# Kernel optimization log

Hardware: AMD Instinct MI355X
Metric: run time of the kernel (lower is better)

The kernel has to match this reference:

```python
import jax, jax.numpy as jnp
import numpy as np

TRACE_LR = 0.1
TRACE_DECAY = 0.99
ERASE_LR = 1.0
EPS = 1e-8


def setup_inputs() -> dict:
    key = jax.random.key(0)
    k1, k2, k3, k4 = jax.random.split(key, 4)
    B, H, S, D = 8, 8, 4096, 64
    DM = 768
    Q = jax.random.normal(k1, (B, H, S, D), dtype=jnp.float32)
    V = jax.random.normal(k2, (B, H, S, D), dtype=jnp.float32)
    # value_traces buffer (small random state so erase path is non-trivial)
    trace = jax.random.normal(k3, (H, D, D), dtype=jnp.float32) * 0.01
    # W_out: Linear(H*D -> DM), weight shape (DM, H*D), out = x @ W.T
    W_out = jax.random.normal(k4, (DM, H * D), dtype=jnp.float32) / np.sqrt(H * D)
    return {"Q": Q, "V": V, "trace": trace, "W_out": W_out}


def _hebbian_write(Q, V, trace):
    """Erase-before-write + decayed Hebbian outer-product update.

    Q, V: (B, H, S, D); trace: (H, D, D). Shift-1 offset: key at i, value at i+2.
    """
    B, H, S, D = Q.shape
    Q_store = Q[:, :, :-2, :]            # (B,H,S-2,D)
    V_store = V[:, :, 2:, :]             # (B,H,S-2,D)
    denom = B * (S - 2)
    # reconsolidation erasure of old associations along normalized keys
    Q_norm = jnp.clip(jnp.linalg.norm(Q_store, axis=-1, keepdims=True), EPS)
    Q_erase = Q_store / Q_norm
    V_old = jnp.einsum('bhip,hpq->bhiq', Q_erase, trace)
    erase = jnp.einsum('bhip,bhiq->hpq', Q_erase, V_old) / denom
    trace = trace - ERASE_LR * erase
    # Hebbian outer-product write
    update = jnp.einsum('bhip,bhiq->hpq', Q_store, V_store) / denom
    return TRACE_DECAY * trace + TRACE_LR * update


def reference(Q, V, trace, W_out):
    B, H, S, D = Q.shape
    new_trace = _hebbian_write(Q, V, trace)
    # shift-1 retrieval: Q_addr at position i uses Q from position i-1
    Q_addr = jnp.concatenate(
        [jnp.zeros_like(Q[:, :, :1, :]), Q[:, :, :-1, :]], axis=2)  # (B,H,S,D)
    V_ret = jnp.einsum('bhsp,hpq->bhsq', Q_addr, new_trace)          # (B,H,S,D)
    V_ret = V_ret.transpose(0, 2, 1, 3).reshape(B, S, H * D)         # (B,S,H*D)
    return V_ret @ W_out.T                                           # (B,S,d_model)
```

## Files before the change

### kernel.cpp

```cpp
#include <hip/hip_runtime.h>

#define B_ 8
#define H_ 8
#define S_ 4096
#define D_ 64
#define DM_ 768
#define NSTORE 4094
#define DENOM 32752.0f

typedef short bfrag_t __attribute__((ext_vector_type(8)));
typedef float f32x4_t __attribute__((ext_vector_type(4)));

__device__ inline unsigned short f2bf(float x) {
    unsigned int u = __float_as_uint(x);
    unsigned int r = (u + 0x7fffu + ((u >> 16) & 1u)) >> 16;
    return (unsigned short)r;
}

__device__ inline unsigned int cvtpk(float lo, float hi) {
    unsigned int r;
    asm("v_cvt_pk_bf16_f32 %0, %1, %2" : "=v"(r) : "v"(lo), "v"(hi));
    return r;
}

__device__ inline void pl16swap(float& a, float& b) {
    asm("v_permlane16_swap_b32 %0, %1" : "+v"(a), "+v"(b));
}
__device__ inline void pl32swap(float& a, float& b) {
    asm("v_permlane32_swap_b32 %0, %1" : "+v"(a), "+v"(b));
}

template <int CTRL>
__device__ inline float dpp_add(float x) {
    int y = __builtin_amdgcn_update_dpp(0, __float_as_int(x), CTRL, 0xf, 0xf, true);
    return x + __int_as_float(y);
}

__device__ inline void async_copy16(const void* g, void* lds) {
    __builtin_amdgcn_global_load_lds((__attribute__((address_space(1))) void*)g,
                                     (__attribute__((address_space(3))) void*)lds,
                                     16, 0, 0);
}

__device__ inline void barrier_lds_only() {
    __builtin_amdgcn_sched_barrier(0);
    asm volatile("s_waitcnt lgkmcnt(0)" ::: "memory");
    __builtin_amdgcn_s_barrier();
    __builtin_amdgcn_sched_barrier(0);
}

#define MFMA16(a, b, c) __builtin_amdgcn_mfma_f32_16x16x32_bf16((a), (b), (c), 0, 0, 0)

template <bool PART>
__global__ __launch_bounds__(256, 4) void gram_kernel(
    const float* __restrict__ Q, const float* __restrict__ V,
    float* __restrict__ gG, float* __restrict__ gU,
    unsigned short* __restrict__ Qbf, float* __restrict__ gP, int writeQbf) {
    const int split = blockIdx.x, h = blockIdx.y, b = blockIdx.z;
    const int nsplit = gridDim.x;
    const int rowsPer = 4096 / nsplit;
    const int nTiles = rowsPer >> 6;
    const int tmask = nTiles - 1;
    const int t = threadIdx.x;
    const int wave = t >> 6, lane = t & 63;
    const int quad = lane >> 4, l15 = lane & 15;
    const int rgrp = t >> 4;
    const int c4 = t & 15;
    __shared__ __align__(16) unsigned short Qs[2][4096];
    __shared__ __align__(16) unsigned short Vs[2][4096];

    const size_t bh = (size_t)(b * H_ + h);
    const float* Qbh = Q + bh * S_ * D_;
    const float* Vbh = V + bh * S_ * D_;
    unsigned short* Qo = Qbf + bh * S_ * D_;

    f32x4_t accG[4] = {}, accU[4] = {};
    const int r0 = split * rowsPer;

    float4 qr[4], vr[4];
    auto loadT = [&](int tile) {
        const int rbase = r0 + tile * 64;
        #pragma unroll
        for (int i = 0; i < 4; ++i) {
            int r = rbase + i * 16 + rgrp;
            qr[i] = *(const float4*)(Qbh + (size_t)r * D_ + c4 * 4);
            vr[i] = (r < NSTORE) ? *(const float4*)(Vbh + (size_t)(r + 2) * D_ + c4 * 4)
                                 : make_float4(0.f, 0.f, 0.f, 0.f);
        }
    };
    auto rd8 = [&](const unsigned short* arr, int p, int gk) {
        const int bx = p & 15;
        uint2 lo = *(const uint2*)&arr[p * 64 + (((gk * 2) ^ bx) << 2)];
        uint2 hi = *(const uint2*)&arr[p * 64 + (((gk * 2 + 1) ^ bx) << 2)];
        union { uint2 u2[2]; bfrag_t f; } u;
        u.u2[0] = lo; u.u2[1] = hi;
        return u.f;
    };

    const int tstart = (split * 3 + h * 5 + b * 7) & tmask;

    loadT(tstart);
    for (int it = 0; it < nTiles; ++it) {
        const int tile = (tstart + it) & tmask;
        const int buf = it & 1;
        const int rbase = r0 + tile * 64;
        unsigned short* Qb_ = Qs[buf];
        unsigned short* Vb_ = Vs[buf];
        #pragma unroll
        for (int i = 0; i < 4; ++i) {
            int r = rbase + i * 16 + rgrp;
            float4 q4 = qr[i], v4 = vr[i];
            if (writeQbf) {
                uint2 u = make_uint2(cvtpk(q4.x, q4.y), cvtpk(q4.z, q4.w));
                *(uint2*)(Qo + (size_t)r * D_ + c4 * 4) = u;
            }
            if (r >= NSTORE) q4 = make_float4(0.f, 0.f, 0.f, 0.f);
            float ss = q4.x * q4.x + q4.y * q4.y + q4.z * q4.z + q4.w * q4.w;
            ss = dpp_add<0xB1>(ss);
            ss = dpp_add<0x4E>(ss);
            ss = dpp_add<0x141>(ss);
            ss = dpp_add<0x140>(ss);
            float sc = fmaxf(ss, 1e-16f);
            float sr = rsqrtf(sc);
            float sv = sc * sr;
            float a0 = q4.x * sr, a1 = q4.y * sr, a2 = q4.z * sr, a3 = q4.w * sr;
            float b0 = v4.x * sv, b1 = v4.y * sv, b2 = v4.z * sv, b3 = v4.w * sv;
            pl16swap(a0, a1); pl16swap(a2, a3);
            pl32swap(a0, a2); pl32swap(a1, a3);
            pl16swap(b0, b1); pl16swap(b2, b3);
            pl32swap(b0, b2); pl32swap(b1, b3);
            const int p = c4 * 4 + quad;
            const int off = p * 64 + (((i * 4 + wave) ^ (p & 15)) << 2);
            *(uint2*)&Qb_[off] = make_uint2(cvtpk(a0, a1), cvtpk(a2, a3));
            *(uint2*)&Vb_[off] = make_uint2(cvtpk(b0, b1), cvtpk(b2, b3));
        }
        if (it + 1 < nTiles) loadT((tstart + it + 1) & tmask);
        barrier_lds_only();
        #pragma unroll
        for (int c = 0; c < 2; ++c) {
            const int gk = c * 4 + quad;
            bfrag_t af = rd8(Qb_, wave * 16 + l15, gk);
            #pragma unroll
            for (int j = 0; j < 4; ++j) {
                bfrag_t bq = rd8(Qb_, j * 16 + l15, gk);
                bfrag_t bv = rd8(Vb_, j * 16 + l15, gk);
                accG[j] = MFMA16(af, bq, accG[j]);
                accU[j] = MFMA16(af, bv, accU[j]);
            }
        }
    }
    if (PART) {
        const int slab = split * 8 + b;
        float* base = gP + ((size_t)(h * 128 + slab) * 2) * 4096;
        #pragma unroll
        for (int j = 0; j < 4; ++j) {
            int coln = j * 16 + l15;
            #pragma unroll
            for (int r = 0; r < 4; ++r) {
                int row = wave * 16 + quad * 4 + r;
                base[row * 64 + coln]        = accG[j][r];
                base[4096 + row * 64 + coln] = accU[j][r];
            }
        }
    } else {
        float* gGh = gG + h * 4096;
        float* gUh = gU + h * 4096;
        #pragma unroll
        for (int j = 0; j < 4; ++j) {
            int coln = j * 16 + l15;
            #pragma unroll
            for (int r = 0; r < 4; ++r) {
                int row = wave * 16 + quad * 4 + r;
                atomicAdd(&gGh[row * 64 + coln], accG[j][r]);
                atomicAdd(&gUh[row * 64 + coln], accU[j][r]);
            }
        }
    }
}

__global__ __launch_bounds__(256) void reduce_kernel(
    const float* __restrict__ gP, float* __restrict__ gG, float* __restrict__ gU) {
    const int h = blockIdx.x, chunk = blockIdx.y, t = threadIdx.x;
    const int arr = t >> 7, idx = chunk * 128 + (t & 127);
    const float* base = gP + ((size_t)(h * 128) * 2 + arr) * 4096 + idx;
    const int slstart = ((h << 4) + (chunk << 2)) & 127;
    float s = 0.f;
    #pragma unroll 8
    for (int i = 0; i < 128; ++i) {
        int sl = (slstart + i) & 127;
        s += base[(size_t)sl * 2 * 4096];
    }
    (arr ? gU : gG)[h * 4096 + idx] = s;
}

__global__ __launch_bounds__(256) void wc_kernel(
    const float* __restrict__ gG, const float* __restrict__ gU,
    const float* __restrict__ trace, const float* __restrict__ Wout,
    unsigned short* __restrict__ WcT) {
    const int nc = blockIdx.x, h = blockIdx.y, t = threadIdx.x;
    __shared__ float Gs[64][68];
    __shared__ float Ts[64][68];
    __shared__ float TsT[64][68];
    __shared__ float WbT[64][132];
    const float* Gh = gG + h * 4096;
    const float* Uh = gU + h * 4096;
    const float* Th = trace + h * 4096;
    #pragma unroll
    for (int k = 0; k < 16; ++k) {
        int e = k * 256 + t;
        Gs[e >> 6][e & 63] = Gh[e];
        Ts[e >> 6][e & 63] = Th[e];
    }
    #pragma unroll
    for (int i = 0; i < 8; ++i) {
        int f = i * 256 + t;
        int n = f >> 4, q4 = f & 15;
        float4 w = *(const float4*)(Wout + (size_t)(nc * 128 + n) * 512 + h * 64 + q4 * 4);
        WbT[q4 * 4 + 0][n] = w.x; WbT[q4 * 4 + 1][n] = w.y;
        WbT[q4 * 4 + 2][n] = w.z; WbT[q4 * 4 + 3][n] = w.w;
    }
    __syncthreads();
    {
        const int p = t >> 2, q0 = (t & 3) * 16;
        f32x4_t acc[4] = {};
        for (int r = 0; r < 64; ++r) {
            float g = Gs[p][r];
            #pragma unroll
            for (int i = 0; i < 4; ++i) {
                f32x4_t tv = *(const f32x4_t*)&Ts[r][q0 + i * 4];
                acc[i] += g * tv;
            }
        }
        const float inv = 1.0f / DENOM;
        #pragma unroll
        for (int i = 0; i < 4; ++i) {
            f32x4_t ts = *(const f32x4_t*)&Ts[p][q0 + i * 4];
            f32x4_t uu = *(const f32x4_t*)(Uh + p * 64 + q0 + i * 4);
            f32x4_t res = 0.99f * (ts - acc[i] * inv) + (0.1f * inv) * uu;
            TsT[q0 + i * 4 + 0][p] = res[0];
            TsT[q0 + i * 4 + 1][p] = res[1];
            TsT[q0 + i * 4 + 2][p] = res[2];
            TsT[q0 + i * 4 + 3][p] = res[3];
        }
    }
    __syncthreads();
    const int n0 = (t >> 4) * 8, p0 = (t & 15) * 4;
    f32x4_t acc[8] = {};
    for (int q = 0; q < 64; ++q) {
        f32x4_t tp = *(const f32x4_t*)&TsT[q][p0];
        f32x4_t w0 = *(const f32x4_t*)&WbT[q][n0];
        f32x4_t w1 = *(const f32x4_t*)&WbT[q][n0 + 4];
        #pragma unroll
        for (int i = 0; i < 4; ++i) acc[i] += w0[i] * tp;
        #pragma unroll
        for (int i = 0; i < 4; ++i) acc[4 + i] += w1[i] * tp;
    }
    #pragma unroll
    for (int i = 0; i < 8; ++i) {
        int n = nc * 128 + n0 + i;
        ushort4 u;
        u.x = f2bf(acc[i][0]); u.y = f2bf(acc[i][1]);
        u.z = f2bf(acc[i][2]); u.w = f2bf(acc[i][3]);
        *(ushort4*)(WcT + (size_t)n * 512 + h * 64 + p0) = u;
    }
}

__global__ __launch_bounds__(256, 3) void matmul_fast(
    const unsigned short* __restrict__ Qb, const unsigned short* __restrict__ WcT,
    float* __restrict__ out) {
    const int mTile = blockIdx.x;
    const int nTile = blockIdx.y;
    const int t = threadIdx.x;
    const int wave = t >> 6, lane = t & 63;
    const int wm = wave >> 1, wn = wave & 1;
    const int quad = lane >> 4, l15 = lane & 15;
    __shared__ __align__(16) unsigned short As[128 * 64];
    __shared__ __align__(16) unsigned short Bs[128 * 64];
    const int b = mTile >> 5;
    const int s0 = (mTile & 31) * 128;
    const int nBase = nTile * 128;
    const int rl8 = lane >> 3, g = lane & 7;
    const int gs = g ^ rl8;
    f32x4_t acc[4][4] = {};

    const int hstart = (mTile * 3 + nTile * 5) & 7;
    for (int hh = 0; hh < 8; ++hh) {
        const int h = (hstart + hh) & 7;
        const unsigned short* Qbh = Qb + (size_t)(b * H_ + h) * S_ * D_;
        #pragma unroll
        for (int k = 0; k < 4; ++k) {
            int ch = wave * 4 + k;
            int row = ch * 8 + rl8;
            int s = s0 + row;
            int sc = (s > 0) ? (s - 1) : 0;
            async_copy16(Qbh + (size_t)sc * 64 + gs * 8, &As[ch * 512 + lane * 8]);
            async_copy16(WcT + (size_t)(nBase + row) * 512 + h * 64 + gs * 8,
                         &Bs[ch * 512 + lane * 8]);
        }
        __syncthreads();
        if (s0 == 0) {
            if (t < 8) ((uint4*)As)[t] = make_uint4(0, 0, 0, 0);
            __syncthreads();
        }
        #pragma unroll
        for (int c = 0; c < 2; ++c) {
            int gk = c * 4 + quad;
            bfrag_t af[4], bf[4];
            #pragma unroll
            for (int i = 0; i < 4; ++i) {
                int row = wm * 64 + i * 16 + l15;
                af[i] = *(const bfrag_t*)&As[row * 64 + ((gk ^ (row & 7)) << 3)];
            }
            #pragma unroll
            for (int j = 0; j < 4; ++j) {
                int row = wn * 64 + j * 16 + l15;
                bf[j] = *(const bfrag_t*)&Bs[row * 64 + ((gk ^ (row & 7)) << 3)];
            }
            #pragma unroll
            for (int i = 0; i < 4; ++i)
                #pragma unroll
                for (int j = 0; j < 4; ++j)
                    acc[i][j] = MFMA16(af[i], bf[j], acc[i][j]);
        }
        __syncthreads();
    }
    const size_t mBase = (size_t)mTile * 128;
    #pragma unroll
    for (int i = 0; i < 4; ++i) {
        int mrow = wm * 64 + i * 16 + quad * 4;
        #pragma unroll
        for (int j = 0; j < 4; ++j) {
            int n = nBase + wn * 64 + j * 16 + l15;
            #pragma unroll
            for (int r = 0; r < 4; ++r)
                out[(mBase + mrow + r) * DM_ + n] = acc[i][j][r];
        }
    }
}

__global__ __launch_bounds__(256, 2) void matmul_f32(
    const float* __restrict__ Qf, const unsigned short* __restrict__ WcT,
    float* __restrict__ out) {
    const int mTile = blockIdx.x, nTile = blockIdx.y;
    const int t = threadIdx.x;
    const int wave = t >> 6, lane = t & 63;
    const int wm = wave >> 1, wn = wave & 1;
    const int quad = lane >> 4, l15 = lane & 15;
    __shared__ __align__(16) unsigned short As[128][72];
    __shared__ __align__(16) unsigned short Bs[128][72];
    const int b = mTile >> 5;
    const int s0 = (mTile & 31) * 128;
    const int nBase = nTile * 128;
    f32x4_t acc[4][4] = {};
    const int hstart = (mTile * 3 + nTile * 5) & 7;
    for (int hh = 0; hh < 8; ++hh) {
        const int h = (hstart + hh) & 7;
        const float* Qbh = Qf + (size_t)(b * H_ + h) * S_ * D_;
        #pragma unroll
        for (int i = 0; i < 8; ++i) {
            int f = i * 256 + t;
            int row = f >> 4, c4 = f & 15;
            int s = s0 + row;
            float4 q4 = make_float4(0.f, 0.f, 0.f, 0.f);
            if (s > 0) q4 = *(const float4*)(Qbh + (size_t)(s - 1) * D_ + c4 * 4);
            ushort4 u;
            u.x = f2bf(q4.x); u.y = f2bf(q4.y); u.z = f2bf(q4.z); u.w = f2bf(q4.w);
            *(ushort4*)(&As[row][c4 * 4]) = u;
        }
        #pragma unroll
        for (int i = 0; i < 4; ++i) {
            int f = i * 256 + t;
            int row = f >> 3, c8 = f & 7;
            uint4 w = *(const uint4*)(WcT + (size_t)(nBase + row) * 512 + h * 64 + c8 * 8);
            *(uint4*)(&Bs[row][c8 * 8]) = w;
        }
        __syncthreads();
        #pragma unroll
        for (int c = 0; c < 2; ++c) {
            int k0 = c * 32 + quad * 8;
            bfrag_t af[4], bf[4];
            #pragma unroll
            for (int i = 0; i < 4; ++i)
                af[i] = *(const bfrag_t*)(&As[wm * 64 + i * 16 + l15][k0]);
            #pragma unroll
            for (int j = 0; j < 4; ++j)
                bf[j] = *(const bfrag_t*)(&Bs[wn * 64 + j * 16 + l15][k0]);
            #pragma unroll
            for (int i = 0; i < 4; ++i)
                #pragma unroll
                for (int j = 0; j < 4; ++j)
                    acc[i][j] = MFMA16(af[i], bf[j], acc[i][j]);
        }
        __syncthreads();
    }
    const size_t mBase = (size_t)mTile * 128;
    #pragma unroll
    for (int i = 0; i < 4; ++i) {
        int mrow = wm * 64 + i * 16 + quad * 4;
        #pragma unroll
        for (int j = 0; j < 4; ++j) {
            int n = nBase + wn * 64 + j * 16 + l15;
            #pragma unroll
            for (int r = 0; r < 4; ++r)
                out[(mBase + mrow + r) * DM_ + n] = acc[i][j][r];
        }
    }
}

extern "C" void kernel_launch(void* const* d_in, const int* in_sizes, int n_in,
                              void* d_out, int out_size, void* d_ws, size_t ws_size,
                              hipStream_t stream) {
    const float* Q     = (const float*)d_in[0];
    const float* V     = (const float*)d_in[1];
    const float* trace = (const float*)d_in[2];
    const float* Wout  = (const float*)d_in[3];
    float* out = (float*)d_out;

    float* gG   = (float*)d_ws;
    float* gU   = gG + 32768;
    float* Tnew = gU + 32768;
    unsigned short* WcT = (unsigned short*)(Tnew + 32768);
    unsigned short* Qbf = WcT + 393216;
    float* gP = (float*)(Qbf + (size_t)B_ * H_ * S_ * D_);

    const size_t needQbf  = 1179648u + 33554432u;
    const size_t needFull = needQbf + 33554432u;
    const int mode = (ws_size >= needFull) ? 2 : ((ws_size >= needQbf) ? 1 : 0);

    if (mode == 2) {
        gram_kernel<true><<<dim3(16, 8, 8), 256, 0, stream>>>(Q, V, gG, gU, Qbf, gP, 1);
        reduce_kernel<<<dim3(8, 32), 256, 0, stream>>>(gP, gG, gU);
    } else {
        hipMemsetAsync(d_ws, 0, 2 * 32768 * sizeof(float), stream);
        gram_kernel<false><<<dim3(8, 8, 8), 256, 0, stream>>>(Q, V, gG, gU, Qbf, gP, mode >= 1);
    }
    wc_kernel<<<dim3(6, 8), 256, 0, stream>>>(gG, gU, trace, Wout, WcT);
    if (mode >= 1)
        matmul_fast<<<dim3(256, 6), 256, 0, stream>>>(Qbf, WcT, out);
    else
        matmul_f32<<<dim3(256, 6), 256, 0, stream>>>(Q, WcT, out);
}
```

Baseline: 265.5 us.

## Drop partial-slab reduction; single-buffer gram kernel with more splits and atomics

Removes the partial-sum workspace path and its separate reduce kernel, so the Gram and update matrices are always accumulated with global atomics after a memset. The gram kernel loses its register prefetch and LDS double buffering: it loads each tile directly and adds a second barrier per tile. It now runs 32 splits per (b,h) with a launch bound raised to 6 blocks per CU. The aim is to hide latency through occupancy instead of software pipelining and to drop the extra kernel and its traffic, at the price of more atomic contention and exposed load latency.

```diff
diff --git a/kernel.cpp b/kernel.cpp
--- a/kernel.cpp
+++ b/kernel.cpp
@@ -51,11 +51,10 @@
 
 #define MFMA16(a, b, c) __builtin_amdgcn_mfma_f32_16x16x32_bf16((a), (b), (c), 0, 0, 0)
 
-template <bool PART>
-__global__ __launch_bounds__(256, 4) void gram_kernel(
+__global__ __launch_bounds__(256, 6) void gram_kernel(
     const float* __restrict__ Q, const float* __restrict__ V,
     float* __restrict__ gG, float* __restrict__ gU,
-    unsigned short* __restrict__ Qbf, float* __restrict__ gP, int writeQbf) {
+    unsigned short* __restrict__ Qbf, int writeQbf) {
     const int split = blockIdx.x, h = blockIdx.y, b = blockIdx.z;
     const int nsplit = gridDim.x;
     const int rowsPer = 4096 / nsplit;
@@ -66,8 +65,8 @@
     const int quad = lane >> 4, l15 = lane & 15;
     const int rgrp = t >> 4;
     const int c4 = t & 15;
-    __shared__ __align__(16) unsigned short Qs[2][4096];
-    __shared__ __align__(16) unsigned short Vs[2][4096];
+    __shared__ __align__(16) unsigned short Qs[4096];
+    __shared__ __align__(16) unsigned short Vs[4096];
 
     const size_t bh = (size_t)(b * H_ + h);
     const float* Qbh = Q + bh * S_ * D_;
@@ -77,17 +76,6 @@
     f32x4_t accG[4] = {}, accU[4] = {};
     const int r0 = split * rowsPer;
 
-    float4 qr[4], vr[4];
-    auto loadT = [&](int tile) {
-        const int rbase = r0 + tile * 64;
-        #pragma unroll
-        for (int i = 0; i < 4; ++i) {
-            int r = rbase + i * 16 + rgrp;
-            qr[i] = *(const float4*)(Qbh + (size_t)r * D_ + c4 * 4);
-            vr[i] = (r < NSTORE) ? *(const float4*)(Vbh + (size_t)(r + 2) * D_ + c4 * 4)
-                                 : make_float4(0.f, 0.f, 0.f, 0.f);
-        }
-    };
     auto rd8 = [&](const unsigned short* arr, int p, int gk) {
         const int bx = p & 15;
         uint2 lo = *(const uint2*)&arr[p * 64 + (((gk * 2) ^ bx) << 2)];
@@ -99,17 +87,16 @@
 
     const int tstart = (split * 3 + h * 5 + b * 7) & tmask;
 
-    loadT(tstart);
     for (int it = 0; it < nTiles; ++it) {
         const int tile = (tstart + it) & tmask;
-        const int buf = it & 1;
         const int rbase = r0 + tile * 64;
-        unsigned short* Qb_ = Qs[buf];
-        unsigned short* Vb_ = Vs[buf];
         #pragma unroll
         for (int i = 0; i < 4; ++i) {
             int r = rbase + i * 16 + rgrp;
-            float4 q4 = qr[i], v4 = vr[i];
+            float4 q4 = *(const float4*)(Qbh + (size_t)r * D_ + c4 * 4);
+            float4 v4 = (r < NSTORE)
+                ? *(const float4*)(Vbh + (size_t)(r + 2) * D_ + c4 * 4)
+                : make_float4(0.f, 0.f, 0.f, 0.f);
             if (writeQbf) {
                 uint2 u = make_uint2(cvtpk(q4.x, q4.y), cvtpk(q4.z, q4.w));
                 *(uint2*)(Qo + (size_t)r * D_ + c4 * 4) = u;
@@ -131,66 +118,36 @@
             pl32swap(b0, b2); pl32swap(b1, b3);
             const int p = c4 * 4 + quad;
             const int off = p * 64 + (((i * 4 + wave) ^ (p & 15)) << 2);
-            *(uint2*)&Qb_[off] = make_uint2(cvtpk(a0, a1), cvtpk(a2, a3));
-            *(uint2*)&Vb_[off] = make_uint2(cvtpk(b0, b1), cvtpk(b2, b3));
-        }
-        if (it + 1 < nTiles) loadT((tstart + it + 1) & tmask);
+            *(uint2*)&Qs[off] = make_uint2(cvtpk(a0, a1), cvtpk(a2, a3));
+            *(uint2*)&Vs[off] = make_uint2(cvtpk(b0, b1), cvtpk(b2, b3));
+        }
         barrier_lds_only();
         #pragma unroll
         for (int c = 0; c < 2; ++c) {
             const int gk = c * 4 + quad;
-            bfrag_t af = rd8(Qb_, wave * 16 + l15, gk);
+            bfrag_t af = rd8(Qs, wave * 16 + l15, gk);
             #pragma unroll
             for (int j = 0; j < 4; ++j) {
-                bfrag_t bq = rd8(Qb_, j * 16 + l15, gk);
-                bfrag_t bv = rd8(Vb_, j * 16 + l15, gk);
+                bfrag_t bq = rd8(Qs, j * 16 + l15, gk);
+                bfrag_t bv = rd8(Vs, j * 16 + l15, gk);
                 accG[j] = MFMA16(af, bq, accG[j]);
                 accU[j] = MFMA16(af, bv, accU[j]);
             }
         }
-    }
-    if (PART) {
-        const int slab = split * 8 + b;
-        float* base = gP + ((size_t)(h * 128 + slab) * 2) * 4096;
-        #pragma unroll
-        for (int j = 0; j < 4; ++j) {
-            int coln = j * 16 + l15;
-            #pragma unroll
-            for (int r = 0; r < 4; ++r) {
-                int row = wave * 16 + quad * 4 + r;
-                base[row * 64 + coln]        = accG[j][r];
-                base[4096 + row * 64 + coln] = accU[j][r];
-            }
-        }
-    } else {
-        float* gGh = gG + h * 4096;
-        float* gUh = gU + h * 4096;
-        #pragma unroll
-        for (int j = 0; j < 4; ++j) {
-            int coln = j * 16 + l15;
-            #pragma unroll
-            for (int r = 0; r < 4; ++r) {
-                int row = wave * 16 + quad * 4 + r;
-                atomicAdd(&gGh[row * 64 + coln], accG[j][r]);
-                atomicAdd(&gUh[row * 64 + coln], accU[j][r]);
-            }
-        }
-    }
-}
-
-__global__ __launch_bounds__(256) void reduce_kernel(
-    const float* __restrict__ gP, float* __restrict__ gG, float* __restrict__ gU) {
-    const int h = blockIdx.x, chunk = blockIdx.y, t = threadIdx.x;
-    const int arr = t >> 7, idx = chunk * 128 + (t & 127);
-    const float* base = gP + ((size_t)(h * 128) * 2 + arr) * 4096 + idx;
-    const int slstart = ((h << 4) + (chunk << 2)) & 127;
-    float s = 0.f;
-    #pragma unroll 8
-    for (int i = 0; i < 128; ++i) {
-        int sl = (slstart + i) & 127;
-        s += base[(size_t)sl * 2 * 4096];
-    }
-    (arr ? gU : gG)[h * 4096 + idx] = s;
+        barrier_lds_only();
+    }
+    float* gGh = gG + h * 4096;
+    float* gUh = gU + h * 4096;
+    #pragma unroll
+    for (int j = 0; j < 4; ++j) {
+        int coln = j * 16 + l15;
+        #pragma unroll
+        for (int r = 0; r < 4; ++r) {
+            int row = wave * 16 + quad * 4 + r;
+            atomicAdd(&gGh[row * 64 + coln], accG[j][r]);
+            atomicAdd(&gUh[row * 64 + coln], accU[j][r]);
+        }
+    }
 }
 
 __global__ __launch_bounds__(256) void wc_kernel(
@@ -418,22 +375,15 @@
 
     float* gG   = (float*)d_ws;
     float* gU   = gG + 32768;
-    float* Tnew = gU + 32768;
-    unsigned short* WcT = (unsigned short*)(Tnew + 32768);
+    float* hole = gU + 32768;
+    unsigned short* WcT = (unsigned short*)(hole + 32768);
     unsigned short* Qbf = WcT + 393216;
-    float* gP = (float*)(Qbf + (size_t)B_ * H_ * S_ * D_);
-
-    const size_t needQbf  = 1179648u + 33554432u;
-    const size_t needFull = needQbf + 33554432u;
-    const int mode = (ws_size >= needFull) ? 2 : ((ws_size >= needQbf) ? 1 : 0);
-
-    if (mode == 2) {
-        gram_kernel<true><<<dim3(16, 8, 8), 256, 0, stream>>>(Q, V, gG, gU, Qbf, gP, 1);
-        reduce_kernel<<<dim3(8, 32), 256, 0, stream>>>(gP, gG, gU);
-    } else {
-        hipMemsetAsync(d_ws, 0, 2 * 32768 * sizeof(float), stream);
-        gram_kernel<false><<<dim3(8, 8, 8), 256, 0, stream>>>(Q, V, gG, gU, Qbf, gP, mode >= 1);
-    }
+
+    const size_t needQbf = 1179648u + 33554432u;
+    const int mode = (ws_size >= needQbf) ? 1 : 0;
+
+    hipMemsetAsync(d_ws, 0, 2 * 32768 * sizeof(float), stream);
+    gram_kernel<<<dim3(32, 8, 8), 256, 0, stream>>>(Q, V, gG, gU, Qbf, mode);
     wc_kernel<<<dim3(6, 8), 256, 0, stream>>>(gG, gU, trace, Wout, WcT);
     if (mode >= 1)
         matmul_fast<<<dim3(256, 6), 256, 0, stream>>>(Qbf, WcT, out);
```

Result: slower. 288.3 us (+8.6%).

## Double-buffer matmul_fast LDS tiles and source zero row from a zeroed buffer

Applied to the files above, without the earlier changes.

matmul_fast now keeps two LDS buffers for the A and B tiles and issues the async global-to-LDS copy for the next head while the current head's MFMAs run. The extra barrier that zeroed the first row is removed by pointing the copy at a small zeroed workspace region instead. This doubles LDS use and lowers the launch-bounds occupancy hint from 3 to 2 blocks, and it adds one small memset per launch.

```diff
diff --git a/kernel.cpp b/kernel.cpp
--- a/kernel.cpp
+++ b/kernel.cpp
@@ -45,6 +45,13 @@
 __device__ inline void barrier_lds_only() {
     __builtin_amdgcn_sched_barrier(0);
     asm volatile("s_waitcnt lgkmcnt(0)" ::: "memory");
+    __builtin_amdgcn_s_barrier();
+    __builtin_amdgcn_sched_barrier(0);
+}
+
+__device__ inline void barrier_vm_drain() {
+    __builtin_amdgcn_sched_barrier(0);
+    asm volatile("s_waitcnt vmcnt(0) lgkmcnt(0)" ::: "memory");
     __builtin_amdgcn_s_barrier();
     __builtin_amdgcn_sched_barrier(0);
 }
@@ -104,8 +111,8 @@
         const int tile = (tstart + it) & tmask;
         const int buf = it & 1;
         const int rbase = r0 + tile * 64;
-        unsigned short* Qb_ = Qs[buf];
-        unsigned short* Vb_ = Vs[buf];
+        unsigned short* Qlds = Qs[buf];
+        unsigned short* Vlds = Vs[buf];
         #pragma unroll
         for (int i = 0; i < 4; ++i) {
             int r = rbase + i * 16 + rgrp;
@@ -131,19 +138,19 @@
             pl32swap(b0, b2); pl32swap(b1, b3);
             const int p = c4 * 4 + quad;
             const int off = p * 64 + (((i * 4 + wave) ^ (p & 15)) << 2);
-            *(uint2*)&Qb_[off] = make_uint2(cvtpk(a0, a1), cvtpk(a2, a3));
-            *(uint2*)&Vb_[off] = make_uint2(cvtpk(b0, b1), cvtpk(b2, b3));
+            *(uint2*)&Qlds[off] = make_uint2(cvtpk(a0, a1), cvtpk(a2, a3));
+            *(uint2*)&Vlds[off] = make_uint2(cvtpk(b0, b1), cvtpk(b2, b3));
         }
         if (it + 1 < nTiles) loadT((tstart + it + 1) & tmask);
         barrier_lds_only();
         #pragma unroll
         for (int c = 0; c < 2; ++c) {
             const int gk = c * 4 + quad;
-            bfrag_t af = rd8(Qb_, wave * 16 + l15, gk);
+            bfrag_t af = rd8(Qlds, wave * 16 + l15, gk);
             #pragma unroll
             for (int j = 0; j < 4; ++j) {
-                bfrag_t bq = rd8(Qb_, j * 16 + l15, gk);
-                bfrag_t bv = rd8(Vb_, j * 16 + l15, gk);
+                bfrag_t bq = rd8(Qlds, j * 16 + l15, gk);
+                bfrag_t bv = rd8(Vlds, j * 16 + l15, gk);
                 accG[j] = MFMA16(af, bq, accG[j]);
                 accU[j] = MFMA16(af, bv, accU[j]);
             }
@@ -265,43 +272,52 @@
     }
 }
 
-__global__ __launch_bounds__(256, 3) void matmul_fast(
+__global__ __launch_bounds__(256, 2) void matmul_fast(
     const unsigned short* __restrict__ Qb, const unsigned short* __restrict__ WcT,
-    float* __restrict__ out) {
+    const unsigned short* __restrict__ zeroSrc, float* __restrict__ out) {
     const int mTile = blockIdx.x;
     const int nTile = blockIdx.y;
     const int t = threadIdx.x;
     const int wave = t >> 6, lane = t & 63;
     const int wm = wave >> 1, wn = wave & 1;
     const int quad = lane >> 4, l15 = lane & 15;
-    __shared__ __align__(16) unsigned short As[128 * 64];
-    __shared__ __align__(16) unsigned short Bs[128 * 64];
+    __shared__ __align__(16) unsigned short As[2][128 * 64];
+    __shared__ __align__(16) unsigned short Bs[2][128 * 64];
     const int b = mTile >> 5;
     const int s0 = (mTile & 31) * 128;
     const int nBase = nTile * 128;
     const int rl8 = lane >> 3, g = lane & 7;
     const int gs = g ^ rl8;
     f32x4_t acc[4][4] = {};
-
     const int hstart = (mTile * 3 + nTile * 5) & 7;
-    for (int hh = 0; hh < 8; ++hh) {
+
+    auto stage = [&](int hh, int buf) {
         const int h = (hstart + hh) & 7;
         const unsigned short* Qbh = Qb + (size_t)(b * H_ + h) * S_ * D_;
+        unsigned short* Ap = &As[buf][0];
+        unsigned short* Bp = &Bs[buf][0];
         #pragma unroll
         for (int k = 0; k < 4; ++k) {
             int ch = wave * 4 + k;
             int row = ch * 8 + rl8;
             int s = s0 + row;
-            int sc = (s > 0) ? (s - 1) : 0;
-            async_copy16(Qbh + (size_t)sc * 64 + gs * 8, &As[ch * 512 + lane * 8]);
+            const unsigned short* srcA = (s > 0)
+                ? Qbh + (size_t)(s - 1) * 64 + gs * 8
+                : zeroSrc + gs * 8;
+            async_copy16(srcA, &Ap[ch * 512 + lane * 8]);
             async_copy16(WcT + (size_t)(nBase + row) * 512 + h * 64 + gs * 8,
-                         &Bs[ch * 512 + lane * 8]);
-        }
-        __syncthreads();
-        if (s0 == 0) {
-            if (t < 8) ((uint4*)As)[t] = make_uint4(0, 0, 0, 0);
-            __syncthreads();
-        }
+                         &Bp[ch * 512 + lane * 8]);
+        }
+    };
+
+    stage(0, 0);
+
+    for (int hh = 0; hh < 8; ++hh) {
+        const int buf = hh & 1;
+        barrier_vm_drain();
+        if (hh + 1 < 8) stage(hh + 1, buf ^ 1);
+        const unsigned short* Ap = &As[buf][0];
+        const unsigned short* Bp = &Bs[buf][0];
         #pragma unroll
         for (int c = 0; c < 2; ++c) {
             int gk = c * 4 + quad;
@@ -309,12 +325,12 @@
             #pragma unroll
             for (int i = 0; i < 4; ++i) {
                 int row = wm * 64 + i * 16 + l15;
-                af[i] = *(const bfrag_t*)&As[row * 64 + ((gk ^ (row & 7)) << 3)];
+                af[i] = *(const bfrag_t*)&Ap[row * 64 + ((gk ^ (row & 7)) << 3)];
             }
             #pragma unroll
             for (int j = 0; j < 4; ++j) {
                 int row = wn * 64 + j * 16 + l15;
-                bf[j] = *(const bfrag_t*)&Bs[row * 64 + ((gk ^ (row & 7)) << 3)];
+                bf[j] = *(const bfrag_t*)&Bp[row * 64 + ((gk ^ (row & 7)) << 3)];
             }
             #pragma unroll
             for (int i = 0; i < 4; ++i)
@@ -322,7 +338,6 @@
                 for (int j = 0; j < 4; ++j)
                     acc[i][j] = MFMA16(af[i], bf[j], acc[i][j]);
         }
-        __syncthreads();
     }
     const size_t mBase = (size_t)mTile * 128;
     #pragma unroll
@@ -418,25 +433,28 @@
 
     float* gG   = (float*)d_ws;
     float* gU   = gG + 32768;
-    float* Tnew = gU + 32768;
-    unsigned short* WcT = (unsigned short*)(Tnew + 32768);
+    float* hole = gU + 32768;
+    unsigned short* WcT = (unsigned short*)(hole + 32768);
     unsigned short* Qbf = WcT + 393216;
     float* gP = (float*)(Qbf + (size_t)B_ * H_ * S_ * D_);
 
     const size_t needQbf  = 1179648u + 33554432u;
     const size_t needFull = needQbf + 33554432u;
     const int mode = (ws_size >= needFull) ? 2 : ((ws_size >= needQbf) ? 1 : 0);
+
+    (void)hipMemsetAsync(hole, 0, 256, stream);
 
     if (mode == 2) {
         gram_kernel<true><<<dim3(16, 8, 8), 256, 0, stream>>>(Q, V, gG, gU, Qbf, gP, 1);
         reduce_kernel<<<dim3(8, 32), 256, 0, stream>>>(gP, gG, gU);
     } else {
-        hipMemsetAsync(d_ws, 0, 2 * 32768 * sizeof(float), stream);
+        (void)hipMemsetAsync(d_ws, 0, 2 * 32768 * sizeof(float), stream);
         gram_kernel<false><<<dim3(8, 8, 8), 256, 0, stream>>>(Q, V, gG, gU, Qbf, gP, mode >= 1);
     }
     wc_kernel<<<dim3(6, 8), 256, 0, stream>>>(gG, gU, trace, Wout, WcT);
     if (mode >= 1)
-        matmul_fast<<<dim3(256, 6), 256, 0, stream>>>(Qbf, WcT, out);
+        matmul_fast<<<dim3(256, 6), 256, 0, stream>>>(Qbf, WcT,
+                                                      (const unsigned short*)hole, out);
     else
         matmul_f32<<<dim3(256, 6), 256, 0, stream>>>(Q, WcT, out);
 }
```

Result: slower. 273.1 us (+2.9%).
